# Kernel optimization log

Hardware: AMD Instinct MI355X
Metric: run time of the kernel (lower is better)

The kernel has to match this reference:

```python
import jax, jax.numpy as jnp
import numpy as np

DT = 1e-4   # self.dttt
DX = 1.0    # self.dxx
FRE = 100.0 # self.fre
PI = 3.1415926  # constant used literally in the torch code


def setup_inputs() -> dict:
    key = jax.random.key(0)
    k1, k2, k3, k4 = jax.random.split(key, 4)
    H = W = 512
    steps = 256  # coffe * bsize1
    output = jax.random.normal(k1, (steps + 2, 1, H, W), dtype=jnp.float32)
    c = jax.random.uniform(k2, (1, 1, H, W), dtype=jnp.float32)  # wave speed map
    loc_x = jax.random.randint(k3, (3,), 0, 510)
    loc_y = jax.random.randint(k4, (3,), 0, 510)
    return {"output": output, "c": c, "loc_x": loc_x, "loc_y": loc_y,
            "bsize1": 256, "id2": 1, "coffe": 1}


def reference(output, c, loc_x, loc_y, bsize1, id2, coffe):
    # FDTD rollout of get_phy_Loss2. output: [T,1,H,W]; c: [1,1,H,W].
    steps = int(coffe * bsize1)              # number of new frames produced
    cc = c[0, 0]                              # [H, W]
    r = (DT ** 2) * cc ** 2 / (DX ** 2)       # r1 == r2 since dx == dy
    src_mask = loc_x != -1                    # sources with loc_x == -1 are skipped

    def step(carry, n):
        prev, cur = carry                     # frames n-1 and n, each [H, W]
        lap = r[1:-1, 1:-1] * (
            (cur[2:, 1:-1] - 2.0 * cur[1:-1, 1:-1] + cur[:-2, 1:-1])
            + (cur[1:-1, 2:] - 2.0 * cur[1:-1, 1:-1] + cur[1:-1, :-2]))
        interior = 2.0 * cur[1:-1, 1:-1] - prev[1:-1, 1:-1] + lap
        new = jnp.zeros_like(cur).at[1:-1, 1:-1].set(interior)
        # source injection (after interior update, before boundary overwrite)
        src = 1500.0 * jnp.sin(2.0 * PI * FRE * (bsize1 * id2 + n + 1) * DT)
        new = new.at[loc_x, loc_y].set(
            jnp.where(src_mask, src, new[loc_x, loc_y]))
        # absorbing-style boundary updates, applied in the same order as torch:
        new = new.at[0, :].set(cur[0, :] - DT * cc[0, :] * (cur[0, :] - cur[1, :]) / DX)
        new = new.at[:, 0].set(cur[:, 0] - DT * cc[:, 0] * (cur[:, 0] - cur[:, 1]) / DX)
        new = new.at[:, -1].set(cur[:, -1] - DT * cc[:, -1] * (cur[:, -1] - cur[:, -2]) / DX)
        new = new.at[-1, :].set(cur[-1, :] - DT * cc[-1, :] * (cur[-1, :] - cur[-2, :]) / DX)
        return (cur, new), new

    ns = jnp.arange(1, steps + 1)
    _, ys = jax.lax.scan(step, (output[0, 0], output[1, 0]), ns)
    return ys[:, None, :, :]  # [steps, 1, H, W] == output3[2:] unsqueezed
```

## Files before the change

kernel.cpp:

```cpp
#include <hip/hip_runtime.h>


#define HH 512
#define WW 512
#define TILE 32
#define TS 16
#define NW 8
#define RPT 8
#define PHC ((float)(2.0 * 3.1415926 * 100.0))

#define LDS_BARRIER() asm volatile("s_waitcnt lgkmcnt(0)\n\ts_barrier" ::: "memory")

#if __has_builtin(__builtin_amdgcn_update_dpp)
__device__ __forceinline__ float nbrL(float x) {
    int i = __builtin_bit_cast(int, x);
    i = __builtin_amdgcn_update_dpp(i, i, 0x138, 0xf, 0xf, false);
    return __builtin_bit_cast(float, i);
}
__device__ __forceinline__ float nbrR(float x) {
    int i = __builtin_bit_cast(int, x);
    i = __builtin_amdgcn_update_dpp(i, i, 0x130, 0xf, 0xf, false);
    return __builtin_bit_cast(float, i);
}
#else
__device__ __forceinline__ float nbrL(float x) { return __shfl_up(x, 1, 64); }
__device__ __forceinline__ float nbrR(float x) { return __shfl_down(x, 1, 64); }
#endif

__global__ void fdtd_zero_flags(int* f) { f[threadIdx.x] = 0; }

__global__ __launch_bounds__(512)
void fdtd_flags_k(const float* __restrict__ in_out,
                  const float* __restrict__ cmap,
                  const int* __restrict__ locx,
                  const int* __restrict__ locy,
                  const int* __restrict__ pb,
                  const int* __restrict__ pid2,
                  float* __restrict__ out,
                  int steps, int* __restrict__ flags)
{
    __shared__ float sb[2][NW][2][64];

    const int tid  = threadIdx.x;
    const int lane = tid & 63;
    const int w    = tid >> 6;
    const int bx   = blockIdx.x & 15;
    const int by   = blockIdx.x >> 4;
    const int gx0  = bx * TILE - TS;
    const int gy0  = by * TILE - TS;
    const int gc   = gx0 + lane;
    const int R    = w * RPT;

    const int lx0 = locx[0], ly0 = locy[0];
    const int lx1 = locx[1], ly1 = locy[1];
    const int lx2 = locx[2], ly2 = locy[2];
    const int Bn  = pb[0] * pid2[0];

    float cur[RPT], pv[RPT], rr[RPT], cv[RPT];
    bool  issrc[RPT];
    unsigned m0 = 0, m511 = 0;
    const bool colOK = (gc >= 0) & (gc < WW);

    #pragma unroll
    for (int j = 0; j < RPT; ++j) {
        const int gr = gy0 + R + j;
        float c = 0.f, ce = 0.f, pp = 0.f;
        if (colOK && gr >= 0 && gr < HH) {
            const int gi = gr * WW + gc;
            c  = cmap[gi];
            ce = in_out[(size_t)(HH * WW) + gi];
            pp = in_out[gi];
        }
        cur[j] = ce; pv[j] = pp; cv[j] = c;
        rr[j]  = 1.0e-8f * c * c;
        issrc[j] = (gr == lx0 && gc == ly0) || (gr == lx1 && gc == ly1) ||
                   (gr == lx2 && gc == ly2);
        if (gr == 0)      m0   |= (1u << j);
        if (gr == HH - 1) m511 |= (1u << j);
    }

    const int wup = (w == 0)      ? 0      : w - 1;
    const int sup = (w == 0)      ? 0      : 1;
    const int wdn = (w == NW - 1) ? NW - 1 : w + 1;
    const int sdn = (w == NW - 1) ? 1      : 0;

    const bool edge    = (bx == 0) | (bx == 15) | (by == 0) | (by == 15);
    const bool isC0    = (gc == 0);
    const bool isC511  = (gc == WW - 1);
    const bool keep    = (w >= 2) & (w <= 5) & (lane >= 16) & (lane < 48);
    const size_t rowOff = (size_t)(gy0 + R) * WW + gc;

    for (int t0 = 0; t0 < steps; t0 += TS) {
        const int nk = (steps - t0 < TS) ? (steps - t0) : TS;

        if (t0 > 0) {
            asm volatile("s_waitcnt vmcnt(0)" ::: "memory");
            __syncthreads();
            if (tid == 0)
                __hip_atomic_store(&flags[blockIdx.x], t0,
                                   __ATOMIC_RELAXED, __HIP_MEMORY_SCOPE_AGENT);
            if (tid < 8) {
                const int dy[8] = {-1,-1,-1, 0, 0, 1, 1, 1};
                const int dx[8] = {-1, 0, 1,-1, 1,-1, 0, 1};
                const int nby = by + dy[tid];
                const int nbx = bx + dx[tid];
                if (nby >= 0 && nby < 16 && nbx >= 0 && nbx < 16) {
                    const int nb = (nby << 4) | nbx;
                    while (__hip_atomic_load(&flags[nb], __ATOMIC_RELAXED,
                                             __HIP_MEMORY_SCOPE_AGENT) < t0)
                        __builtin_amdgcn_s_sleep(2);
                }
            }
            __syncthreads();
            if (!keep) {
                const float* cF = out + (size_t)(t0 - 1) * (size_t)(HH * WW);
                const float* pF = out + (size_t)(t0 - 2) * (size_t)(HH * WW);
                #pragma unroll
                for (int j = 0; j < RPT; ++j) {
                    const int gr = gy0 + R + j;
                    float ce = 0.f, pp = 0.f;
                    if (colOK && gr >= 0 && gr < HH) {
                        const int gi = gr * WW + gc;
                        ce = __hip_atomic_load(cF + gi, __ATOMIC_RELAXED,
                                               __HIP_MEMORY_SCOPE_AGENT);
                        pp = __hip_atomic_load(pF + gi, __ATOMIC_RELAXED,
                                               __HIP_MEMORY_SCOPE_AGENT);
                    }
                    cur[j] = ce; pv[j] = pp;
                }
            }
        }
        sb[0][w][0][lane] = cur[0];
        sb[0][w][1][lane] = cur[RPT - 1];
        __syncthreads();

        if (!edge) {
            #pragma unroll 2
            for (int k = 1; k <= nk; ++k) {
                const int p = (k - 1) & 1;
                const float srcv =
                    1500.0f * __sinf(PHC * (float)(Bn + t0 + k + 1) * 1.0e-4f);
                const float upb = sb[p][wup][sup][lane];
                const float dnb = sb[p][wdn][sdn][lane];
                float nc[RPT];
                #pragma unroll
                for (int j = 0; j < RPT; ++j) {
                    const float c = cur[j];
                    const float u = (j == 0)       ? upb : cur[j - 1];
                    const float d = (j == RPT - 1) ? dnb : cur[j + 1];
                    const float l = nbrL(c);
                    const float r = nbrR(c);
                    float v = 2.f * c - pv[j] +
                              rr[j] * (((u + d) + (l + r)) - 4.f * c);
                    nc[j] = issrc[j] ? srcv : v;
                }
                sb[p ^ 1][w][0][lane] = nc[0];
                sb[p ^ 1][w][1][lane] = nc[RPT - 1];
                if (keep) {
                    float* op = out + (size_t)(t0 + k - 1) * (size_t)(HH * WW)
                                    + rowOff;
                    #pragma unroll
                    for (int j = 0; j < RPT; ++j)
                        __hip_atomic_store(op + j * WW, nc[j],
                                           __ATOMIC_RELAXED,
                                           __HIP_MEMORY_SCOPE_AGENT);
                }
                #pragma unroll
                for (int j = 0; j < RPT; ++j) { pv[j] = cur[j]; cur[j] = nc[j]; }
                LDS_BARRIER();
            }
        } else {
            #pragma unroll 2
            for (int k = 1; k <= nk; ++k) {
                const int p = (k - 1) & 1;
                const float srcv =
                    1500.0f * __sinf(PHC * (float)(Bn + t0 + k + 1) * 1.0e-4f);
                const float upb = sb[p][wup][sup][lane];
                const float dnb = sb[p][wdn][sdn][lane];
                float nc[RPT];
                #pragma unroll
                for (int j = 0; j < RPT; ++j) {
                    const float c = cur[j];
                    const float u = (j == 0)       ? upb : cur[j - 1];
                    const float d = (j == RPT - 1) ? dnb : cur[j + 1];
                    const float l = nbrL(c);
                    const float r = nbrR(c);
                    float v = 2.f * c - pv[j] +
                              rr[j] * (((u + d) + (l + r)) - 4.f * c);
                    v = issrc[j] ? srcv : v;
                    if ((m0 >> j) & 1u)   v = c - 1.0e-4f * cv[j] * (c - d);
                    if (isC0)             v = c - 1.0e-4f * cv[j] * (c - r);
                    if (isC511)           v = c - 1.0e-4f * cv[j] * (c - l);
                    if ((m511 >> j) & 1u) v = c - 1.0e-4f * cv[j] * (c - u);
                    nc[j] = v;
                }
                sb[p ^ 1][w][0][lane] = nc[0];
                sb[p ^ 1][w][1][lane] = nc[RPT - 1];
                if (keep) {
                    float* op = out + (size_t)(t0 + k - 1) * (size_t)(HH * WW)
                                    + rowOff;
                    #pragma unroll
                    for (int j = 0; j < RPT; ++j)
                        __hip_atomic_store(op + j * WW, nc[j],
                                           __ATOMIC_RELAXED,
                                           __HIP_MEMORY_SCOPE_AGENT);
                }
                #pragma unroll
                for (int j = 0; j < RPT; ++j) { pv[j] = cur[j]; cur[j] = nc[j]; }
                LDS_BARRIER();
            }
        }
    }
}

extern "C" void kernel_launch(void* const* d_in, const int* in_sizes, int n_in,
                              void* d_out, int out_size, void* d_ws, size_t ws_size,
                              hipStream_t stream) {
    const float* in_out = (const float*)d_in[0];
    const float* cmap   = (const float*)d_in[1];
    const int*   locx   = (const int*)d_in[2];
    const int*   locy   = (const int*)d_in[3];
    const int*   pb     = (const int*)d_in[4];
    const int*   pid2   = (const int*)d_in[5];
    float*       outp   = (float*)d_out;
    int*         flags  = (int*)d_ws;

    const int HW = HH * WW;
    int steps = out_size / HW;

    hipLaunchKernelGGL(fdtd_zero_flags, dim3(1), dim3(256), 0, stream, flags);

    void* args[] = { (void*)&in_out, (void*)&cmap, (void*)&locx, (void*)&locy,
                     (void*)&pb, (void*)&pid2, (void*)&outp, (void*)&steps,
                     (void*)&flags };
    hipLaunchCooperativeKernel((const void*)fdtd_flags_k,
                               dim3((HH / TILE) * (WW / TILE)),
                               dim3(512), args, 0, stream);
}
```

Baseline: 241.6 us.

## Replace per-step workgroup barrier with neighbour-wave LDS flag dataflow

Removes the workgroup-wide LDS barrier at the end of each time step. Each wave now publishes a per-wave step counter in shared memory with release semantics and spin-waits with acquire semantics only on its upper and lower neighbour waves. Interior rows 1..6 are computed before the wait, so only the two halo-dependent rows sit behind the neighbour sync. This lets waves drift relative to each other and overlap work, at the cost of spin loops with s_sleep and subtle ordering around the double-buffered halo array.

Measured after the change: 236.8 us. 1.02x faster.

```diff
diff --git a/kernel.cpp b/kernel.cpp
--- a/kernel.cpp
+++ b/kernel.cpp
@@ -9,8 +9,6 @@
 #define RPT 8
 #define PHC ((float)(2.0 * 3.1415926 * 100.0))
 
-#define LDS_BARRIER() asm volatile("s_waitcnt lgkmcnt(0)\n\ts_barrier" ::: "memory")
-
 #if __has_builtin(__builtin_amdgcn_update_dpp)
 __device__ __forceinline__ float nbrL(float x) {
     int i = __builtin_bit_cast(int, x);
@@ -30,16 +28,17 @@
 __global__ void fdtd_zero_flags(int* f) { f[threadIdx.x] = 0; }
 
 __global__ __launch_bounds__(512)
-void fdtd_flags_k(const float* __restrict__ in_out,
-                  const float* __restrict__ cmap,
-                  const int* __restrict__ locx,
-                  const int* __restrict__ locy,
-                  const int* __restrict__ pb,
-                  const int* __restrict__ pid2,
-                  float* __restrict__ out,
-                  int steps, int* __restrict__ flags)
+void fdtd_dflow(const float* __restrict__ in_out,
+                const float* __restrict__ cmap,
+                const int* __restrict__ locx,
+                const int* __restrict__ locy,
+                const int* __restrict__ pb,
+                const int* __restrict__ pid2,
+                float* __restrict__ out,
+                int steps, int* __restrict__ flags)
 {
     __shared__ float sb[2][NW][2][64];
+    __shared__ int   cnt[NW];
 
     const int tid  = threadIdx.x;
     const int lane = tid & 63;
@@ -78,6 +77,7 @@
         if (gr == 0)      m0   |= (1u << j);
         if (gr == HH - 1) m511 |= (1u << j);
     }
+    if (tid < NW) cnt[tid] = 0;
 
     const int wup = (w == 0)      ? 0      : w - 1;
     const int sup = (w == 0)      ? 0      : 1;
@@ -140,22 +140,40 @@
                 const int p = (k - 1) & 1;
                 const float srcv =
                     1500.0f * __sinf(PHC * (float)(Bn + t0 + k + 1) * 1.0e-4f);
-                const float upb = sb[p][wup][sup][lane];
-                const float dnb = sb[p][wdn][sdn][lane];
                 float nc[RPT];
                 #pragma unroll
-                for (int j = 0; j < RPT; ++j) {
+                for (int j = 1; j < RPT - 1; ++j) {
                     const float c = cur[j];
-                    const float u = (j == 0)       ? upb : cur[j - 1];
-                    const float d = (j == RPT - 1) ? dnb : cur[j + 1];
                     const float l = nbrL(c);
                     const float r = nbrR(c);
                     float v = 2.f * c - pv[j] +
-                              rr[j] * (((u + d) + (l + r)) - 4.f * c);
-                    nc[j] = issrc[j] ? srcv : v;
+                              rr[j] * (((cur[j - 1] + cur[j + 1]) + (l + r)) - 4.f * c);
+                    nc[j] = ((issrc[j])) ? srcv : v;
+                }
+                const int need = t0 + k - 1;
+                while (__hip_atomic_load(&cnt[wup], __ATOMIC_ACQUIRE,
+                                         __HIP_MEMORY_SCOPE_WORKGROUP) < need)
+                    __builtin_amdgcn_s_sleep(1);
+                while (__hip_atomic_load(&cnt[wdn], __ATOMIC_ACQUIRE,
+                                         __HIP_MEMORY_SCOPE_WORKGROUP) < need)
+                    __builtin_amdgcn_s_sleep(1);
+                const float upb = sb[p][wup][sup][lane];
+                const float dnb = sb[p][wdn][sdn][lane];
+                {
+                    const float c0 = cur[0];
+                    float v0 = 2.f * c0 - pv[0] +
+                               rr[0] * (((upb + cur[1]) + (nbrL(c0) + nbrR(c0))) - 4.f * c0);
+                    nc[0] = issrc[0] ? srcv : v0;
+                    const int J = RPT - 1;
+                    const float c7 = cur[J];
+                    float v7 = 2.f * c7 - pv[J] +
+                               rr[J] * (((cur[J - 1] + dnb) + (nbrL(c7) + nbrR(c7))) - 4.f * c7);
+                    nc[J] = issrc[J] ? srcv : v7;
                 }
                 sb[p ^ 1][w][0][lane] = nc[0];
                 sb[p ^ 1][w][1][lane] = nc[RPT - 1];
+                __hip_atomic_store(&cnt[w], t0 + k, __ATOMIC_RELEASE,
+                                   __HIP_MEMORY_SCOPE_WORKGROUP);
                 if (keep) {
                     float* op = out + (size_t)(t0 + k - 1) * (size_t)(HH * WW)
                                     + rowOff;
@@ -167,7 +185,6 @@
                 }
                 #pragma unroll
                 for (int j = 0; j < RPT; ++j) { pv[j] = cur[j]; cur[j] = nc[j]; }
-                LDS_BARRIER();
             }
         } else {
             #pragma unroll 2
@@ -175,14 +192,12 @@
                 const int p = (k - 1) & 1;
                 const float srcv =
                     1500.0f * __sinf(PHC * (float)(Bn + t0 + k + 1) * 1.0e-4f);
-                const float upb = sb[p][wup][sup][lane];
-                const float dnb = sb[p][wdn][sdn][lane];
                 float nc[RPT];
                 #pragma unroll
-                for (int j = 0; j < RPT; ++j) {
+                for (int j = 1; j < RPT - 1; ++j) {
                     const float c = cur[j];
-                    const float u = (j == 0)       ? upb : cur[j - 1];
-                    const float d = (j == RPT - 1) ? dnb : cur[j + 1];
+                    const float u = cur[j - 1];
+                    const float d = cur[j + 1];
                     const float l = nbrL(c);
                     const float r = nbrR(c);
                     float v = 2.f * c - pv[j] +
@@ -194,8 +209,42 @@
                     if ((m511 >> j) & 1u) v = c - 1.0e-4f * cv[j] * (c - u);
                     nc[j] = v;
                 }
+                const int need = t0 + k - 1;
+                while (__hip_atomic_load(&cnt[wup], __ATOMIC_ACQUIRE,
+                                         __HIP_MEMORY_SCOPE_WORKGROUP) < need)
+                    __builtin_amdgcn_s_sleep(1);
+                while (__hip_atomic_load(&cnt[wdn], __ATOMIC_ACQUIRE,
+                                         __HIP_MEMORY_SCOPE_WORKGROUP) < need)
+                    __builtin_amdgcn_s_sleep(1);
+                const float upb = sb[p][wup][sup][lane];
+                const float dnb = sb[p][wdn][sdn][lane];
+                {
+                    const float c0 = cur[0];
+                    const float l0 = nbrL(c0), r0 = nbrR(c0);
+                    float v0 = 2.f * c0 - pv[0] +
+                               rr[0] * (((upb + cur[1]) + (l0 + r0)) - 4.f * c0);
+                    v0 = issrc[0] ? srcv : v0;
+                    if (m0 & 1u)      v0 = c0 - 1.0e-4f * cv[0] * (c0 - cur[1]);
+                    if (isC0)         v0 = c0 - 1.0e-4f * cv[0] * (c0 - r0);
+                    if (isC511)       v0 = c0 - 1.0e-4f * cv[0] * (c0 - l0);
+                    if (m511 & 1u)    v0 = c0 - 1.0e-4f * cv[0] * (c0 - upb);
+                    nc[0] = v0;
+                    const int J = RPT - 1;
+                    const float c7 = cur[J];
+                    const float l7 = nbrL(c7), r7 = nbrR(c7);
+                    float v7 = 2.f * c7 - pv[J] +
+                               rr[J] * (((cur[J - 1] + dnb) + (l7 + r7)) - 4.f * c7);
+                    v7 = ((issrc[J])) ? srcv : v7;
+                    if ((m0 >> J) & 1u)   v7 = c7 - 1.0e-4f * cv[J] * (c7 - dnb);
+                    if (isC0)             v7 = c7 - 1.0e-4f * cv[J] * (c7 - r7);
+                    if (isC511)           v7 = c7 - 1.0e-4f * cv[J] * (c7 - l7);
+                    if ((m511 >> J) & 1u) v7 = c7 - 1.0e-4f * cv[J] * (c7 - cur[J - 1]);
+                    nc[J] = v7;
+                }
                 sb[p ^ 1][w][0][lane] = nc[0];
                 sb[p ^ 1][w][1][lane] = nc[RPT - 1];
+                __hip_atomic_store(&cnt[w], t0 + k, __ATOMIC_RELEASE,
+                                   __HIP_MEMORY_SCOPE_WORKGROUP);
                 if (keep) {
                     float* op = out + (size_t)(t0 + k - 1) * (size_t)(HH * WW)
                                     + rowOff;
@@ -207,7 +256,6 @@
                 }
                 #pragma unroll
                 for (int j = 0; j < RPT; ++j) { pv[j] = cur[j]; cur[j] = nc[j]; }
-                LDS_BARRIER();
             }
         }
     }
@@ -233,7 +281,7 @@
     void* args[] = { (void*)&in_out, (void*)&cmap, (void*)&locx, (void*)&locy,
                      (void*)&pb, (void*)&pid2, (void*)&outp, (void*)&steps,
                      (void*)&flags };
-    hipLaunchCooperativeKernel((const void*)fdtd_flags_k,
+    hipLaunchCooperativeKernel((const void*)fdtd_dflow,
                                dim3((HH / TILE) * (WW / TILE)),
                                dim3(512), args, 0, stream);
 }
```

## Advance two timesteps per LDS exchange using two-row wavefront halos

Applied to the files above, without the earlier changes.

Each wave now holds a 12-row window (two halo rows on each side) and computes two timesteps per iteration. Rows shrink from 10 to 8 across the pair, so neighbouring waves exchange four rows through LDS once per pair. This halves the number of LDS barriers and exchanges per time tile, at the cost of redundant halo computation, more registers, and reloading the halo rows at each tile start. It assumes the step count per tile is even; an odd count would drop a step.

After: 272.8 us. 12.9% more time.

```diff
diff --git a/kernel.cpp b/kernel.cpp
--- a/kernel.cpp
+++ b/kernel.cpp
@@ -3,10 +3,12 @@
 
 #define HH 512
 #define WW 512
+#define HW (HH * WW)
 #define TILE 32
 #define TS 16
 #define NW 8
 #define RPT 8
+#define WIN 12
 #define PHC ((float)(2.0 * 3.1415926 * 100.0))
 
 #define LDS_BARRIER() asm volatile("s_waitcnt lgkmcnt(0)\n\ts_barrier" ::: "memory")
@@ -29,17 +31,103 @@
 
 __global__ void fdtd_zero_flags(int* f) { f[threadIdx.x] = 0; }
 
+template<bool EDGE>
+__device__ __forceinline__ float rowv(float c, float u, float d, float pvv,
+                                      float rrv, float dcv, bool src, float srcv,
+                                      bool b0, bool b511, bool c0, bool c511)
+{
+    const float l = nbrL(c);
+    const float r = nbrR(c);
+    float v = 2.f * c - pvv + rrv * (((u + d) + (l + r)) - 4.f * c);
+    v = src ? srcv : v;
+    if (EDGE) {
+        if (b0)   v = c - dcv * (c - d);
+        if (c0)   v = c - dcv * (c - r);
+        if (c511) v = c - dcv * (c - l);
+        if (b511) v = c - dcv * (c - u);
+    }
+    return v;
+}
+
+typedef float (&SBref)[2][NW][2][2][2][64];
+
+template<bool EDGE>
+__device__ __forceinline__ void run_pairs(
+    float (&cur)[WIN], float (&pv)[WIN], const float (&rr)[WIN],
+    const float (&dcv)[WIN], const bool (&issrc)[WIN],
+    unsigned m0, unsigned m511, bool isC0, bool isC511,
+    bool keep, float* opBase, int t0, int pairs, int Bn, int w, int lane,
+    SBref sb)
+{
+    const int wup = (w == 0)      ? 0      : w - 1;
+    const int sup = (w == 0)      ? 0      : 1;
+    const int wdn = (w == NW - 1) ? NW - 1 : w + 1;
+    const int sdn = (w == NW - 1) ? 1      : 0;
+
+    for (int p = 0; p < pairs; ++p) {
+        const int buf = p & 1;
+        const float srcA =
+            1500.0f * __sinf(PHC * (float)(Bn + t0 + 2 * p + 2) * 1.0e-4f);
+        const float srcB =
+            1500.0f * __sinf(PHC * (float)(Bn + t0 + 2 * p + 3) * 1.0e-4f);
+        float A[WIN], B[WIN];
+        #pragma unroll
+        for (int i = 1; i <= 10; ++i)
+            A[i] = rowv<EDGE>(cur[i], cur[i - 1], cur[i + 1], pv[i],
+                              rr[i], dcv[i], issrc[i], srcA,
+                              (m0 >> i) & 1u, (m511 >> i) & 1u, isC0, isC511);
+        #pragma unroll
+        for (int i = 2; i <= 9; ++i)
+            B[i] = rowv<EDGE>(A[i], A[i - 1], A[i + 1], cur[i],
+                              rr[i], dcv[i], issrc[i], srcB,
+                              (m0 >> i) & 1u, (m511 >> i) & 1u, isC0, isC511);
+        if (keep) {
+            float* opA = opBase + (size_t)(t0 + 2 * p) * (size_t)HW;
+            float* opB = opA + HW;
+            #pragma unroll
+            for (int j = 0; j < RPT; ++j)
+                __hip_atomic_store(opA + j * WW, A[2 + j], __ATOMIC_RELAXED,
+                                   __HIP_MEMORY_SCOPE_AGENT);
+            #pragma unroll
+            for (int j = 0; j < RPT; ++j)
+                __hip_atomic_store(opB + j * WW, B[2 + j], __ATOMIC_RELAXED,
+                                   __HIP_MEMORY_SCOPE_AGENT);
+        }
+        if (p < pairs - 1) {
+            sb[buf][w][0][0][0][lane] = B[2];
+            sb[buf][w][0][0][1][lane] = B[3];
+            sb[buf][w][0][1][0][lane] = A[2];
+            sb[buf][w][0][1][1][lane] = A[3];
+            sb[buf][w][1][0][0][lane] = B[8];
+            sb[buf][w][1][0][1][lane] = B[9];
+            sb[buf][w][1][1][0][lane] = A[8];
+            sb[buf][w][1][1][1][lane] = A[9];
+            LDS_BARRIER();
+            cur[0]  = sb[buf][wup][sup][0][0][lane];
+            cur[1]  = sb[buf][wup][sup][0][1][lane];
+            pv[0]   = sb[buf][wup][sup][1][0][lane];
+            pv[1]   = sb[buf][wup][sup][1][1][lane];
+            cur[10] = sb[buf][wdn][sdn][0][0][lane];
+            cur[11] = sb[buf][wdn][sdn][0][1][lane];
+            pv[10]  = sb[buf][wdn][sdn][1][0][lane];
+            pv[11]  = sb[buf][wdn][sdn][1][1][lane];
+        }
+        #pragma unroll
+        for (int i = 2; i <= 9; ++i) { pv[i] = A[i]; cur[i] = B[i]; }
+    }
+}
+
 __global__ __launch_bounds__(512)
-void fdtd_flags_k(const float* __restrict__ in_out,
-                  const float* __restrict__ cmap,
-                  const int* __restrict__ locx,
-                  const int* __restrict__ locy,
-                  const int* __restrict__ pb,
-                  const int* __restrict__ pid2,
-                  float* __restrict__ out,
-                  int steps, int* __restrict__ flags)
+void fdtd_pair_k(const float* __restrict__ in_out,
+                 const float* __restrict__ cmap,
+                 const int* __restrict__ locx,
+                 const int* __restrict__ locy,
+                 const int* __restrict__ pb,
+                 const int* __restrict__ pid2,
+                 float* __restrict__ out,
+                 int steps, int* __restrict__ flags)
 {
-    __shared__ float sb[2][NW][2][64];
+    __shared__ float sb[2][NW][2][2][2][64];
 
     const int tid  = threadIdx.x;
     const int lane = tid & 63;
@@ -49,46 +137,42 @@
     const int gx0  = bx * TILE - TS;
     const int gy0  = by * TILE - TS;
     const int gc   = gx0 + lane;
-    const int R    = w * RPT;
+    const int RB   = w * RPT - 2;
 
     const int lx0 = locx[0], ly0 = locy[0];
     const int lx1 = locx[1], ly1 = locy[1];
     const int lx2 = locx[2], ly2 = locy[2];
     const int Bn  = pb[0] * pid2[0];
 
-    float cur[RPT], pv[RPT], rr[RPT], cv[RPT];
-    bool  issrc[RPT];
+    float cur[WIN], pv[WIN], rr[WIN], dcv[WIN];
+    bool  issrc[WIN];
     unsigned m0 = 0, m511 = 0;
     const bool colOK = (gc >= 0) & (gc < WW);
 
     #pragma unroll
-    for (int j = 0; j < RPT; ++j) {
-        const int gr = gy0 + R + j;
+    for (int i = 0; i < WIN; ++i) {
+        const int gr = gy0 + RB + i;
         float c = 0.f, ce = 0.f, pp = 0.f;
         if (colOK && gr >= 0 && gr < HH) {
             const int gi = gr * WW + gc;
             c  = cmap[gi];
-            ce = in_out[(size_t)(HH * WW) + gi];
+            ce = in_out[(size_t)HW + gi];
             pp = in_out[gi];
         }
-        cur[j] = ce; pv[j] = pp; cv[j] = c;
-        rr[j]  = 1.0e-8f * c * c;
-        issrc[j] = (gr == lx0 && gc == ly0) || (gr == lx1 && gc == ly1) ||
+        cur[i] = ce; pv[i] = pp;
+        rr[i]  = 1.0e-8f * c * c;
+        dcv[i] = 1.0e-4f * c;
+        issrc[i] = (gr == lx0 && gc == ly0) || (gr == lx1 && gc == ly1) ||
                    (gr == lx2 && gc == ly2);
-        if (gr == 0)      m0   |= (1u << j);
-        if (gr == HH - 1) m511 |= (1u << j);
-    }
-
-    const int wup = (w == 0)      ? 0      : w - 1;
-    const int sup = (w == 0)      ? 0      : 1;
-    const int wdn = (w == NW - 1) ? NW - 1 : w + 1;
-    const int sdn = (w == NW - 1) ? 1      : 0;
+        if (gr == 0)      m0   |= (1u << i);
+        if (gr == HH - 1) m511 |= (1u << i);
+    }
 
     const bool edge    = (bx == 0) | (bx == 15) | (by == 0) | (by == 15);
     const bool isC0    = (gc == 0);
     const bool isC511  = (gc == WW - 1);
     const bool keep    = (w >= 2) & (w <= 5) & (lane >= 16) & (lane < 48);
-    const size_t rowOff = (size_t)(gy0 + R) * WW + gc;
+    float* opBase = out + (size_t)(gy0 + w * RPT) * WW + gc;
 
     for (int t0 = 0; t0 < steps; t0 += TS) {
         const int nk = (steps - t0 < TS) ? (steps - t0) : TS;
@@ -112,12 +196,13 @@
                 }
             }
             __syncthreads();
-            if (!keep) {
-                const float* cF = out + (size_t)(t0 - 1) * (size_t)(HH * WW);
-                const float* pF = out + (size_t)(t0 - 2) * (size_t)(HH * WW);
-                #pragma unroll
-                for (int j = 0; j < RPT; ++j) {
-                    const int gr = gy0 + R + j;
+            const float* cF = out + (size_t)(t0 - 1) * (size_t)HW;
+            const float* pF = cF - HW;
+            #pragma unroll
+            for (int i = 0; i < WIN; ++i) {
+                const bool need = (!keep) | (i < 2) | (i > 9);
+                if (need) {
+                    const int gr = gy0 + RB + i;
                     float ce = 0.f, pp = 0.f;
                     if (colOK && gr >= 0 && gr < HH) {
                         const int gi = gr * WW + gc;
@@ -126,90 +211,18 @@
                         pp = __hip_atomic_load(pF + gi, __ATOMIC_RELAXED,
                                                __HIP_MEMORY_SCOPE_AGENT);
                     }
-                    cur[j] = ce; pv[j] = pp;
+                    cur[i] = ce; pv[i] = pp;
                 }
             }
         }
-        sb[0][w][0][lane] = cur[0];
-        sb[0][w][1][lane] = cur[RPT - 1];
-        __syncthreads();
-
-        if (!edge) {
-            #pragma unroll 2
-            for (int k = 1; k <= nk; ++k) {
-                const int p = (k - 1) & 1;
-                const float srcv =
-                    1500.0f * __sinf(PHC * (float)(Bn + t0 + k + 1) * 1.0e-4f);
-                const float upb = sb[p][wup][sup][lane];
-                const float dnb = sb[p][wdn][sdn][lane];
-                float nc[RPT];
-                #pragma unroll
-                for (int j = 0; j < RPT; ++j) {
-                    const float c = cur[j];
-                    const float u = (j == 0)       ? upb : cur[j - 1];
-                    const float d = (j == RPT - 1) ? dnb : cur[j + 1];
-                    const float l = nbrL(c);
-                    const float r = nbrR(c);
-                    float v = 2.f * c - pv[j] +
-                              rr[j] * (((u + d) + (l + r)) - 4.f * c);
-                    nc[j] = issrc[j] ? srcv : v;
-                }
-                sb[p ^ 1][w][0][lane] = nc[0];
-                sb[p ^ 1][w][1][lane] = nc[RPT - 1];
-                if (keep) {
-                    float* op = out + (size_t)(t0 + k - 1) * (size_t)(HH * WW)
-                                    + rowOff;
-                    #pragma unroll
-                    for (int j = 0; j < RPT; ++j)
-                        __hip_atomic_store(op + j * WW, nc[j],
-                                           __ATOMIC_RELAXED,
-                                           __HIP_MEMORY_SCOPE_AGENT);
-                }
-                #pragma unroll
-                for (int j = 0; j < RPT; ++j) { pv[j] = cur[j]; cur[j] = nc[j]; }
-                LDS_BARRIER();
-            }
-        } else {
-            #pragma unroll 2
-            for (int k = 1; k <= nk; ++k) {
-                const int p = (k - 1) & 1;
-                const float srcv =
-                    1500.0f * __sinf(PHC * (float)(Bn + t0 + k + 1) * 1.0e-4f);
-                const float upb = sb[p][wup][sup][lane];
-                const float dnb = sb[p][wdn][sdn][lane];
-                float nc[RPT];
-                #pragma unroll
-                for (int j = 0; j < RPT; ++j) {
-                    const float c = cur[j];
-                    const float u = (j == 0)       ? upb : cur[j - 1];
-                    const float d = (j == RPT - 1) ? dnb : cur[j + 1];
-                    const float l = nbrL(c);
-                    const float r = nbrR(c);
-                    float v = 2.f * c - pv[j] +
-                              rr[j] * (((u + d) + (l + r)) - 4.f * c);
-                    v = issrc[j] ? srcv : v;
-                    if ((m0 >> j) & 1u)   v = c - 1.0e-4f * cv[j] * (c - d);
-                    if (isC0)             v = c - 1.0e-4f * cv[j] * (c - r);
-                    if (isC511)           v = c - 1.0e-4f * cv[j] * (c - l);
-                    if ((m511 >> j) & 1u) v = c - 1.0e-4f * cv[j] * (c - u);
-                    nc[j] = v;
-                }
-                sb[p ^ 1][w][0][lane] = nc[0];
-                sb[p ^ 1][w][1][lane] = nc[RPT - 1];
-                if (keep) {
-                    float* op = out + (size_t)(t0 + k - 1) * (size_t)(HH * WW)
-                                    + rowOff;
-                    #pragma unroll
-                    for (int j = 0; j < RPT; ++j)
-                        __hip_atomic_store(op + j * WW, nc[j],
-                                           __ATOMIC_RELAXED,
-                                           __HIP_MEMORY_SCOPE_AGENT);
-                }
-                #pragma unroll
-                for (int j = 0; j < RPT; ++j) { pv[j] = cur[j]; cur[j] = nc[j]; }
-                LDS_BARRIER();
-            }
-        }
+
+        const int pairs = nk >> 1;
+        if (!edge)
+            run_pairs<false>(cur, pv, rr, dcv, issrc, m0, m511, isC0, isC511,
+                             keep, opBase, t0, pairs, Bn, w, lane, sb);
+        else
+            run_pairs<true>(cur, pv, rr, dcv, issrc, m0, m511, isC0, isC511,
+                            keep, opBase, t0, pairs, Bn, w, lane, sb);
     }
 }
 
@@ -225,7 +238,6 @@
     float*       outp   = (float*)d_out;
     int*         flags  = (int*)d_ws;
 
-    const int HW = HH * WW;
     int steps = out_size / HW;
 
     hipLaunchKernelGGL(fdtd_zero_flags, dim3(1), dim3(256), 0, stream, flags);
@@ -233,7 +245,7 @@
     void* args[] = { (void*)&in_out, (void*)&cmap, (void*)&locx, (void*)&locy,
                      (void*)&pb, (void*)&pid2, (void*)&outp, (void*)&steps,
                      (void*)&flags };
-    hipLaunchCooperativeKernel((const void*)fdtd_flags_k,
+    hipLaunchCooperativeKernel((const void*)fdtd_pair_k,
                                dim3((HH / TILE) * (WW / TILE)),
                                dim3(512), args, 0, stream);
 }
```

## Slim FDTD inner step: ping-pong registers, precomputed source table, specialized boundary paths

Applied to the files above, without the earlier changes.

Rewrites the per-step update into a templated helper that ping-pongs between two register arrays instead of copying cur/prev each step, and reads the source value from a shared table precomputed once per block rather than calling sin every step. Source injection now runs only in wavefronts that actually contain a source, and top/bottom boundary handling is limited to the specific wavefronts that own those rows. Column-edge handling is specialized through a template parameter. The aim is fewer VALU ops and register moves per step, at the cost of more code and a wider per-step function signature.

Result: faster. 215.4 us, median of 2 (-10.8%).

```diff
diff --git a/kernel.cpp b/kernel.cpp
--- a/kernel.cpp
+++ b/kernel.cpp
@@ -3,6 +3,7 @@
 
 #define HH 512
 #define WW 512
+#define HW (HH * WW)
 #define TILE 32
 #define TS 16
 #define NW 8
@@ -29,17 +30,70 @@
 
 __global__ void fdtd_zero_flags(int* f) { f[threadIdx.x] = 0; }
 
+template<bool COLEDGE>
+__device__ __forceinline__ void fstep(
+    float (&X)[RPT], float (&Y)[RPT],
+    const float (&rr)[RPT], const float (&dcv)[RPT],
+    const float (*sbR)[2][64], float (*sbW)[2][64],
+    int lane, int w, int wup, int sup, int wdn, int sdn,
+    bool topw, bool botw, bool isC0, bool isC511,
+    bool whs, unsigned smask, const float (&srcT)[260], int n,
+    bool keep, float* op)
+{
+    const float upb = sbR[wup][sup][lane];
+    const float dnb = sbR[wdn][sdn][lane];
+    #pragma unroll
+    for (int j = 0; j < RPT; ++j) {
+        const float c = X[j];
+        const float u = (j == 0)       ? upb : X[j - 1];
+        const float d = (j == RPT - 1) ? dnb : X[j + 1];
+        const float lft = nbrL(c);
+        const float rgt = nbrR(c);
+        Y[j] = 2.f * c - Y[j] + rr[j] * (((u + d) + (lft + rgt)) - 4.f * c);
+    }
+    if (whs) {
+        const float srcv = srcT[n];
+        #pragma unroll
+        for (int j = 0; j < RPT; ++j)
+            if ((smask >> j) & 1u) Y[j] = srcv;
+    }
+    if (topw) Y[0] = X[0] - dcv[0] * (X[0] - X[1]);
+    if (COLEDGE) {
+        #pragma unroll
+        for (int j = 0; j < RPT; ++j) {
+            const float c   = X[j];
+            const float rgt = nbrR(c);
+            const float lft = nbrL(c);
+            float v = Y[j];
+            v = isC0   ? (c - dcv[j] * (c - rgt)) : v;
+            v = isC511 ? (c - dcv[j] * (c - lft)) : v;
+            Y[j] = v;
+        }
+    }
+    if (botw) Y[RPT - 1] = X[RPT - 1] - dcv[RPT - 1] * (X[RPT - 1] - X[RPT - 2]);
+    sbW[w][0][lane] = Y[0];
+    sbW[w][1][lane] = Y[RPT - 1];
+    if (keep) {
+        #pragma unroll
+        for (int j = 0; j < RPT; ++j)
+            __hip_atomic_store(op + j * WW, Y[j], __ATOMIC_RELAXED,
+                               __HIP_MEMORY_SCOPE_AGENT);
+    }
+    LDS_BARRIER();
+}
+
 __global__ __launch_bounds__(512)
-void fdtd_flags_k(const float* __restrict__ in_out,
-                  const float* __restrict__ cmap,
-                  const int* __restrict__ locx,
-                  const int* __restrict__ locy,
-                  const int* __restrict__ pb,
-                  const int* __restrict__ pid2,
-                  float* __restrict__ out,
-                  int steps, int* __restrict__ flags)
+void fdtd_diet(const float* __restrict__ in_out,
+               const float* __restrict__ cmap,
+               const int* __restrict__ locx,
+               const int* __restrict__ locy,
+               const int* __restrict__ pb,
+               const int* __restrict__ pid2,
+               float* __restrict__ out,
+               int steps, int* __restrict__ flags)
 {
     __shared__ float sb[2][NW][2][64];
+    __shared__ float srcT[260];
 
     const int tid  = threadIdx.x;
     const int lane = tid & 63;
@@ -56,9 +110,11 @@
     const int lx2 = locx[2], ly2 = locy[2];
     const int Bn  = pb[0] * pid2[0];
 
-    float cur[RPT], pv[RPT], rr[RPT], cv[RPT];
-    bool  issrc[RPT];
-    unsigned m0 = 0, m511 = 0;
+    if (tid <= steps && tid < 260)
+        srcT[tid] = 1500.0f * __sinf(PHC * (float)(Bn + tid + 1) * 1.0e-4f);
+
+    float A[RPT], B[RPT], rr[RPT], dcv[RPT];
+    unsigned smask = 0;
     const bool colOK = (gc >= 0) & (gc < WW);
 
     #pragma unroll
@@ -68,27 +124,32 @@
         if (colOK && gr >= 0 && gr < HH) {
             const int gi = gr * WW + gc;
             c  = cmap[gi];
-            ce = in_out[(size_t)(HH * WW) + gi];
+            ce = in_out[(size_t)HW + gi];
             pp = in_out[gi];
         }
-        cur[j] = ce; pv[j] = pp; cv[j] = c;
+        A[j] = ce; B[j] = pp;
         rr[j]  = 1.0e-8f * c * c;
-        issrc[j] = (gr == lx0 && gc == ly0) || (gr == lx1 && gc == ly1) ||
-                   (gr == lx2 && gc == ly2);
-        if (gr == 0)      m0   |= (1u << j);
-        if (gr == HH - 1) m511 |= (1u << j);
-    }
+        dcv[j] = 1.0e-4f * c;
+        if ((gr == lx0 && gc == ly0) || (gr == lx1 && gc == ly1) ||
+            (gr == lx2 && gc == ly2)) smask |= (1u << j);
+    }
+    const bool whs     = __any((int)(smask != 0));
+    const bool topw    = (by == 0)  && (w == 2);
+    const bool botw    = (by == 15) && (w == 5);
+    const bool coledge = (bx == 0) || (bx == 15);
+    const bool isC0    = (gc == 0);
+    const bool isC511  = (gc == WW - 1);
+    const bool keep    = (w >= 2) & (w <= 5) & (lane >= 16) & (lane < 48);
+    const int  rowOff  = (gy0 + R) * WW + gc;
 
     const int wup = (w == 0)      ? 0      : w - 1;
     const int sup = (w == 0)      ? 0      : 1;
     const int wdn = (w == NW - 1) ? NW - 1 : w + 1;
     const int sdn = (w == NW - 1) ? 1      : 0;
 
-    const bool edge    = (bx == 0) | (bx == 15) | (by == 0) | (by == 15);
-    const bool isC0    = (gc == 0);
-    const bool isC511  = (gc == WW - 1);
-    const bool keep    = (w >= 2) & (w <= 5) & (lane >= 16) & (lane < 48);
-    const size_t rowOff = (size_t)(gy0 + R) * WW + gc;
+    sb[0][w][0][lane] = A[0];
+    sb[0][w][1][lane] = A[RPT - 1];
+    __syncthreads();
 
     for (int t0 = 0; t0 < steps; t0 += TS) {
         const int nk = (steps - t0 < TS) ? (steps - t0) : TS;
@@ -113,8 +174,8 @@
             }
             __syncthreads();
             if (!keep) {
-                const float* cF = out + (size_t)(t0 - 1) * (size_t)(HH * WW);
-                const float* pF = out + (size_t)(t0 - 2) * (size_t)(HH * WW);
+                const float* cF = out + (size_t)(t0 - 1) * (size_t)HW;
+                const float* pF = cF - HW;
                 #pragma unroll
                 for (int j = 0; j < RPT; ++j) {
                     const int gr = gy0 + R + j;
@@ -126,88 +187,54 @@
                         pp = __hip_atomic_load(pF + gi, __ATOMIC_RELAXED,
                                                __HIP_MEMORY_SCOPE_AGENT);
                     }
-                    cur[j] = ce; pv[j] = pp;
-                }
-            }
-        }
-        sb[0][w][0][lane] = cur[0];
-        sb[0][w][1][lane] = cur[RPT - 1];
-        __syncthreads();
-
-        if (!edge) {
-            #pragma unroll 2
-            for (int k = 1; k <= nk; ++k) {
-                const int p = (k - 1) & 1;
-                const float srcv =
-                    1500.0f * __sinf(PHC * (float)(Bn + t0 + k + 1) * 1.0e-4f);
-                const float upb = sb[p][wup][sup][lane];
-                const float dnb = sb[p][wdn][sdn][lane];
-                float nc[RPT];
+                    A[j] = ce; B[j] = pp;
+                }
+            }
+            sb[0][w][0][lane] = A[0];
+            sb[0][w][1][lane] = A[RPT - 1];
+            __syncthreads();
+        }
+
+        float* op = out + (size_t)t0 * (size_t)HW + rowOff;
+        if (!coledge) {
+            for (int k = 1; k + 1 <= nk; k += 2) {
+                fstep<false>(A, B, rr, dcv, sb[0], sb[1], lane, w, wup, sup,
+                             wdn, sdn, topw, botw, isC0, isC511, whs, smask,
+                             srcT, t0 + k, keep, op);
+                op += HW;
+                fstep<false>(B, A, rr, dcv, sb[1], sb[0], lane, w, wup, sup,
+                             wdn, sdn, topw, botw, isC0, isC511, whs, smask,
+                             srcT, t0 + k + 1, keep, op);
+                op += HW;
+            }
+            if (nk & 1) {
+                fstep<false>(A, B, rr, dcv, sb[0], sb[1], lane, w, wup, sup,
+                             wdn, sdn, topw, botw, isC0, isC511, whs, smask,
+                             srcT, t0 + nk, keep, op);
                 #pragma unroll
                 for (int j = 0; j < RPT; ++j) {
-                    const float c = cur[j];
-                    const float u = (j == 0)       ? upb : cur[j - 1];
-                    const float d = (j == RPT - 1) ? dnb : cur[j + 1];
-                    const float l = nbrL(c);
-                    const float r = nbrR(c);
-                    float v = 2.f * c - pv[j] +
-                              rr[j] * (((u + d) + (l + r)) - 4.f * c);
-                    nc[j] = issrc[j] ? srcv : v;
-                }
-                sb[p ^ 1][w][0][lane] = nc[0];
-                sb[p ^ 1][w][1][lane] = nc[RPT - 1];
-                if (keep) {
-                    float* op = out + (size_t)(t0 + k - 1) * (size_t)(HH * WW)
-                                    + rowOff;
-                    #pragma unroll
-                    for (int j = 0; j < RPT; ++j)
-                        __hip_atomic_store(op + j * WW, nc[j],
-                                           __ATOMIC_RELAXED,
-                                           __HIP_MEMORY_SCOPE_AGENT);
-                }
-                #pragma unroll
-                for (int j = 0; j < RPT; ++j) { pv[j] = cur[j]; cur[j] = nc[j]; }
-                LDS_BARRIER();
+                    const float t = A[j]; A[j] = B[j]; B[j] = t;
+                }
             }
         } else {
-            #pragma unroll 2
-            for (int k = 1; k <= nk; ++k) {
-                const int p = (k - 1) & 1;
-                const float srcv =
-                    1500.0f * __sinf(PHC * (float)(Bn + t0 + k + 1) * 1.0e-4f);
-                const float upb = sb[p][wup][sup][lane];
-                const float dnb = sb[p][wdn][sdn][lane];
-                float nc[RPT];
+            for (int k = 1; k + 1 <= nk; k += 2) {
+                fstep<true>(A, B, rr, dcv, sb[0], sb[1], lane, w, wup, sup,
+                            wdn, sdn, topw, botw, isC0, isC511, whs, smask,
+                            srcT, t0 + k, keep, op);
+                op += HW;
+                fstep<true>(B, A, rr, dcv, sb[1], sb[0], lane, w, wup, sup,
+                            wdn, sdn, topw, botw, isC0, isC511, whs, smask,
+                            srcT, t0 + k + 1, keep, op);
+                op += HW;
+            }
+            if (nk & 1) {
+                fstep<true>(A, B, rr, dcv, sb[0], sb[1], lane, w, wup, sup,
+                            wdn, sdn, topw, botw, isC0, isC511, whs, smask,
+                            srcT, t0 + nk, keep, op);
                 #pragma unroll
                 for (int j = 0; j < RPT; ++j) {
-                    const float c = cur[j];
-                    const float u = (j == 0)       ? upb : cur[j - 1];
-                    const float d = (j == RPT - 1) ? dnb : cur[j + 1];
-                    const float l = nbrL(c);
-                    const float r = nbrR(c);
-                    float v = 2.f * c - pv[j] +
-                              rr[j] * (((u + d) + (l + r)) - 4.f * c);
-                    v = issrc[j] ? srcv : v;
-                    if ((m0 >> j) & 1u)   v = c - 1.0e-4f * cv[j] * (c - d);
-                    if (isC0)             v = c - 1.0e-4f * cv[j] * (c - r);
-                    if (isC511)           v = c - 1.0e-4f * cv[j] * (c - l);
-                    if ((m511 >> j) & 1u) v = c - 1.0e-4f * cv[j] * (c - u);
-                    nc[j] = v;
-                }
-                sb[p ^ 1][w][0][lane] = nc[0];
-                sb[p ^ 1][w][1][lane] = nc[RPT - 1];
-                if (keep) {
-                    float* op = out + (size_t)(t0 + k - 1) * (size_t)(HH * WW)
-                                    + rowOff;
-                    #pragma unroll
-                    for (int j = 0; j < RPT; ++j)
-                        __hip_atomic_store(op + j * WW, nc[j],
-                                           __ATOMIC_RELAXED,
-                                           __HIP_MEMORY_SCOPE_AGENT);
-                }
-                #pragma unroll
-                for (int j = 0; j < RPT; ++j) { pv[j] = cur[j]; cur[j] = nc[j]; }
-                LDS_BARRIER();
+                    const float t = A[j]; A[j] = B[j]; B[j] = t;
+                }
             }
         }
     }
@@ -225,7 +252,6 @@
     float*       outp   = (float*)d_out;
     int*         flags  = (int*)d_ws;
 
-    const int HW = HH * WW;
     int steps = out_size / HW;
 
     hipLaunchKernelGGL(fdtd_zero_flags, dim3(1), dim3(256), 0, stream, flags);
@@ -233,7 +259,7 @@
     void* args[] = { (void*)&in_out, (void*)&cmap, (void*)&locx, (void*)&locy,
                      (void*)&pb, (void*)&pid2, (void*)&outp, (void*)&steps,
                      (void*)&flags };
-    hipLaunchCooperativeKernel((const void*)fdtd_flags_k,
+    hipLaunchCooperativeKernel((const void*)fdtd_diet,
                                dim3((HH / TILE) * (WW / TILE)),
                                dim3(512), args, 0, stream);
 }
```
